# Kernel optimization log

Hardware: AMD Instinct MI355X
Metric: run time of the kernel (lower is better)

Reference implementation:

```python
import math
import jax, jax.numpy as jnp
import numpy as np

B, T, H = 4096, 49, 512

def setup_inputs() -> dict:
    key = jax.random.key(0)
    ks = jax.random.split(key, 13)
    sc = 1.0 / math.sqrt(H)
    return {
        "v": jax.random.normal(ks[0], (B, T, H), dtype=jnp.float32),
        "h": jax.random.normal(ks[1], (B, H), dtype=jnp.float32),
        "s": jax.random.normal(ks[2], (B, H), dtype=jnp.float32),
        "W_h": jax.random.normal(ks[3], (H, H), dtype=jnp.float32) * sc,
        "b_h": jax.random.normal(ks[4], (H,), dtype=jnp.float32) * sc,
        "W_v": jax.random.normal(ks[5], (H, H), dtype=jnp.float32) * sc,
        "b_v": jax.random.normal(ks[6], (H,), dtype=jnp.float32) * sc,
        "w_z": jax.random.normal(ks[7], (H,), dtype=jnp.float32) * sc,
        "b_z": jax.random.normal(ks[8], (), dtype=jnp.float32) * sc,
        "W_s": jax.random.normal(ks[9], (H, H), dtype=jnp.float32) * sc,
        "b_s": jax.random.normal(ks[10], (H,), dtype=jnp.float32) * sc,
        "w_beta": jax.random.normal(ks[11], (H,), dtype=jnp.float32) * sc,
        "b_beta": jax.random.normal(ks[12], (), dtype=jnp.float32) * sc,
    }

def reference(v, h, s, W_h, b_h, W_v, b_v, w_z, b_z, W_s, b_s, w_beta, b_beta):
    # eval mode: dropout is identity
    h_proj = h @ W_h + b_h                                  # [B, H]
    v_proj = jnp.einsum('bth,hk->btk', v, W_v) + b_v        # [B, T, H]
    z = jnp.tanh(h_proj[:, None, :] + v_proj)               # [B, T, H]
    z = jnp.einsum('bth,h->bt', z, w_z) + b_z               # [B, T]
    beta = jnp.tanh((s @ W_s + b_s + h_proj) * math.sqrt(0.5))  # [B, H]
    beta = (beta @ w_beta + b_beta)[:, None]                # [B, 1]
    a = jax.nn.softmax(jnp.concatenate([z, beta], axis=1), axis=1)  # [B, T+1]
    v_ext = jnp.concatenate([v, s[:, None, :]], axis=1)     # [B, T+1, H]
    c = jnp.einsum('bt,bth->bh', a, v_ext)                  # [B, H]
    return c
```

## Files before the change

kernel.cpp:

```cpp
#include <hip/hip_runtime.h>
#include <stdint.h>

#define B_ 4096
#define T_ 49
#define H_ 512
#define BT_ (B_*T_)
#define BB 16

typedef __bf16 bf16x8 __attribute__((ext_vector_type(8)));
typedef float  f32x4  __attribute__((ext_vector_type(4)));
typedef unsigned short ushort_;

__device__ __forceinline__ ushort_ f2bf(float f){
  unsigned int u = __float_as_uint(f);
  u += 0x7fffu + ((u >> 16) & 1u);
  return (ushort_)(u >> 16);
}

__device__ __forceinline__ float fast_tanh(float x){
  float e = __expf(2.0f * x);
  return 1.0f - 2.0f * __builtin_amdgcn_rcpf(e + 1.0f);
}

__global__ __launch_bounds__(256) void k_pack(const float* __restrict__ W,
                                              ushort_* __restrict__ pack){
  int idx = blockIdx.x * 256 + threadIdx.x;
  int lane = idx & 63;
  int gt   = (idx >> 6) & 31;
  int kk   = idx >> 11;
  int col  = gt*16 + (lane & 15);
  int k0   = kk*32 + (lane >> 4)*8;
  ushort4 lo, hi;
  lo.x = f2bf(W[(k0+0)*H_ + col]);
  lo.y = f2bf(W[(k0+1)*H_ + col]);
  lo.z = f2bf(W[(k0+2)*H_ + col]);
  lo.w = f2bf(W[(k0+3)*H_ + col]);
  hi.x = f2bf(W[(k0+4)*H_ + col]);
  hi.y = f2bf(W[(k0+5)*H_ + col]);
  hi.z = f2bf(W[(k0+6)*H_ + col]);
  hi.w = f2bf(W[(k0+7)*H_ + col]);
  ushort4* dst = (ushort4*)pack;
  dst[idx*2]   = lo;
  dst[idx*2+1] = hi;
}

__global__ __launch_bounds__(256) void k_proj2(
    const float* __restrict__ h, const float* __restrict__ s,
    const ushort_* __restrict__ whp, const ushort_* __restrict__ wsp,
    const float* __restrict__ bh, const float* __restrict__ bs,
    const float* __restrict__ bv, const float* __restrict__ wbeta,
    const float* __restrict__ bbeta_p,
    float* __restrict__ hpb, float* __restrict__ beta)
{
  __shared__ __align__(16) ushort_ hl[16*H_];
  __shared__ __align__(16) ushort_ sl[16*H_];
  __shared__ float zwp[4][16];
  const int tid = threadIdx.x;
  const int w = tid >> 6, lane = tid & 63;
  const int l15 = lane & 15, l4 = lane >> 4;
  const int b0 = blockIdx.x * 16;

  {
    const int r = tid >> 4;
    const float4* hsrc = (const float4*)(h + (size_t)(b0+r)*H_);
    const float4* ssrc = (const float4*)(s + (size_t)(b0+r)*H_);
    #pragma unroll
    for(int p=0;p<8;p++){
      int q  = (tid & 15) + p*16;
      int k0 = q*4;
      float4 fh = hsrc[q];
      float4 fs = ssrc[q];
      int idx = (k0>>5)*512 + ((((k0&31)>>3)<<4) + r)*8 + (k0&7);
      ushort4 uh; uh.x=f2bf(fh.x); uh.y=f2bf(fh.y); uh.z=f2bf(fh.z); uh.w=f2bf(fh.w);
      ushort4 us; us.x=f2bf(fs.x); us.y=f2bf(fs.y); us.z=f2bf(fs.z); us.w=f2bf(fs.w);
      *(ushort4*)&hl[idx] = uh;
      *(ushort4*)&sl[idx] = us;
    }
  }
  __syncthreads();

  const bf16x8* __restrict__ bph = (const bf16x8*)whp;
  const bf16x8* __restrict__ bps = (const bf16x8*)wsp;
  const int bbase = w*512 + lane;

  f32x4 acch[8], accs[8];
  #pragma unroll
  for(int ni=0;ni<8;ni++){ acch[ni]=(f32x4){0,0,0,0}; accs[ni]=(f32x4){0,0,0,0}; }

  #pragma unroll 2
  for(int kk=0;kk<16;kk++){
    bf16x8 ah = *(const bf16x8*)&hl[kk*512 + lane*8];
    bf16x8 as2 = *(const bf16x8*)&sl[kk*512 + lane*8];
    #pragma unroll
    for(int ni=0;ni<8;ni++){
      acch[ni] = __builtin_amdgcn_mfma_f32_16x16x32_bf16(ah,  bph[kk*2048 + bbase + ni*64], acch[ni], 0,0,0);
      accs[ni] = __builtin_amdgcn_mfma_f32_16x16x32_bf16(as2, bps[kk*2048 + bbase + ni*64], accs[ni], 0,0,0);
    }
  }

  float bhv[8], bsv[8], bvv[8], wbv[8];
  #pragma unroll
  for(int ni=0;ni<8;ni++){
    int col = w*128 + ni*16 + l15;
    bhv[ni] = bh[col]; bsv[ni] = bs[col]; bvv[ni] = bv[col]; wbv[ni] = wbeta[col];
  }
  float btsum[4];
  #pragma unroll
  for(int rr=0;rr<4;rr++){
    int row = l4*4 + rr;
    float bsum = 0.f;
    #pragma unroll
    for(int ni=0;ni<8;ni++){
      int col = w*128 + ni*16 + l15;
      float hp = acch[ni][rr] + bhv[ni];
      hpb[(size_t)(b0+row)*H_ + col] = hp + bvv[ni];
      float bt = fast_tanh((accs[ni][rr] + bsv[ni] + hp) * 0.70710678118654752f);
      bsum = fmaf(bt, wbv[ni], bsum);
    }
    btsum[rr] = bsum;
  }
  #pragma unroll
  for(int rr=0;rr<4;rr++){
    btsum[rr] += __shfl_xor(btsum[rr], 1);
    btsum[rr] += __shfl_xor(btsum[rr], 2);
    btsum[rr] += __shfl_xor(btsum[rr], 4);
    btsum[rr] += __shfl_xor(btsum[rr], 8);
    if(l15 == 0) zwp[w][l4*4+rr] = btsum[rr];
  }
  __syncthreads();
  if(tid < 16)
    beta[b0+tid] = zwp[0][tid] + zwp[1][tid] + zwp[2][tid] + zwp[3][tid] + bbeta_p[0];
}

__global__ __launch_bounds__(256, 2) void k_fused(
    const float* __restrict__ v, const ushort_* __restrict__ bpack,
    const float* __restrict__ hpb, const float* __restrict__ wz,
    const float* __restrict__ bz_p, const float* __restrict__ beta,
    const float* __restrict__ s, float* __restrict__ out)
{
  __shared__ __align__(16) ushort_ Av[49*512];
  __shared__ float zw[4][64];
  __shared__ float a_s[64];
  const int tid = threadIdx.x;
  const int w = tid >> 6, lane = tid & 63;
  const int l15 = lane & 15, l4 = lane >> 4;
  const int b = blockIdx.x;

  const f32x4* __restrict__ vsrc = (const f32x4*)(v + (size_t)b * T_ * H_);
  const bf16x8* __restrict__ bp = (const bf16x8*)bpack;
  const int bbase = w*256 + lane;

  const int srow = tid >> 4, c4 = tid & 15;
  const int slot = ((c4 >> 1) ^ (srow & 7));
  const int wsub = ((c4 & 1) << 3);
  const bool r48 = (tid < 16);

#define VLOAD(N0,N1,N2,N3, CH) { \
    N0 = __builtin_nontemporal_load(vsrc + (srow     )*128 + (CH)*16 + c4); \
    N1 = __builtin_nontemporal_load(vsrc + (srow + 16)*128 + (CH)*16 + c4); \
    N2 = __builtin_nontemporal_load(vsrc + (srow + 32)*128 + (CH)*16 + c4); \
    if(r48) N3 = __builtin_nontemporal_load(vsrc + 48*128 + (CH)*16 + c4); }

#define SWRITE(N0,N1,N2,N3, CH) { \
    const int cb_ = (CH)*128; ushort4 u_; \
    u_.x=f2bf(N0[0]); u_.y=f2bf(N0[1]); u_.z=f2bf(N0[2]); u_.w=f2bf(N0[3]); \
    *(ushort4*)((char*)Av + (srow   )*1024 + cb_ + (slot<<4) + wsub) = u_; \
    u_.x=f2bf(N1[0]); u_.y=f2bf(N1[1]); u_.z=f2bf(N1[2]); u_.w=f2bf(N1[3]); \
    *(ushort4*)((char*)Av + (srow+16)*1024 + cb_ + (slot<<4) + wsub) = u_; \
    u_.x=f2bf(N2[0]); u_.y=f2bf(N2[1]); u_.z=f2bf(N2[2]); u_.w=f2bf(N2[3]); \
    *(ushort4*)((char*)Av + (srow+32)*1024 + cb_ + (slot<<4) + wsub) = u_; \
    if(r48){ \
      u_.x=f2bf(N3[0]); u_.y=f2bf(N3[1]); u_.z=f2bf(N3[2]); u_.w=f2bf(N3[3]); \
      *(ushort4*)((char*)Av + 48*1024 + cb_ + (slot<<4) + wsub) = u_; } }

#define AFRAG(af, KS) { \
    _Pragma("unroll") \
    for(int mi=0;mi<4;mi++){ \
      int row_ = (mi < 3) ? (mi*16 + l15) : 48; \
      int g_   = ((KS)*4 + l4) ^ (row_ & 7); \
      af[mi] = *(const bf16x8*)((const char*)Av + row_*1024 + (g_<<4)); } }

#define MFMA16(af, bfr) { \
    __builtin_amdgcn_s_setprio(1); \
    _Pragma("unroll") \
    for(int mi=0;mi<4;mi++) \
      _Pragma("unroll") \
      for(int ni=0;ni<4;ni++) \
        acc[mi][ni] = __builtin_amdgcn_mfma_f32_16x16x32_bf16(af[mi], bfr[ni], acc[mi][ni], 0,0,0); \
    __builtin_amdgcn_s_setprio(0); }

  f32x4 A0,A1,A2,A3, B0,B1,B2,B3;
  f32x4 acc[4][4];
  #pragma unroll
  for(int mi=0;mi<4;mi++)
    #pragma unroll
    for(int ni=0;ni<4;ni++) acc[mi][ni] = (f32x4){0.f,0.f,0.f,0.f};

  VLOAD(A0,A1,A2,A3, 0)
  SWRITE(A0,A1,A2,A3, 0)
  VLOAD(A0,A1,A2,A3, 1)
  VLOAD(B0,B1,B2,B3, 2)

  bf16x8 ba[4], bb[4], af[4];
  #pragma unroll
  for(int ni=0;ni<4;ni++) ba[ni] = bp[bbase + ni*64];
  __syncthreads();

#define BODY(C, W0,W1,W2,W3) { \
    _Pragma("unroll") \
    for(int ni=0;ni<4;ni++) bb[ni] = bp[(2*(C)+1)*2048 + bbase + ni*64]; \
    AFRAG(af, 2*(C)) \
    MFMA16(af, ba) \
    if((C) < 7){ SWRITE(W0,W1,W2,W3, (C)+1) } \
    if((C) < 5){ VLOAD(W0,W1,W2,W3, (C)+3) } \
    if((C) < 7){ \
      _Pragma("unroll") \
      for(int ni=0;ni<4;ni++) ba[ni] = bp[(2*(C)+2)*2048 + bbase + ni*64]; } \
    AFRAG(af, 2*(C)+1) \
    MFMA16(af, bb) \
    __syncthreads(); }

  #pragma unroll 1
  for(int cc=0; cc<4; cc++){
    const int c0 = 2*cc;
    BODY(c0,   A0,A1,A2,A3)
    BODY(c0+1, B0,B1,B2,B3)
  }

  {
    float wzv[4], hp0[4];
    #pragma unroll
    for(int ni=0;ni<4;ni++){
      int col = w*64 + ni*16 + l15;
      wzv[ni] = wz[col];
      hp0[ni] = hpb[(size_t)b*H_ + col];
    }
    float zp[16];
    #pragma unroll
    for(int mi=0;mi<4;mi++)
      #pragma unroll
      for(int r=0;r<4;r++){
        float az = 0.f;
        #pragma unroll
        for(int ni=0;ni<4;ni++)
          az = fmaf(fast_tanh(acc[mi][ni][r] + hp0[ni]), wzv[ni], az);
        zp[mi*4+r] = az;
      }
    #pragma unroll
    for(int i=0;i<16;i++){
      zp[i] += __shfl_xor(zp[i], 1);
      zp[i] += __shfl_xor(zp[i], 2);
      zp[i] += __shfl_xor(zp[i], 4);
      zp[i] += __shfl_xor(zp[i], 8);
    }
    if(l15 == 0){
      #pragma unroll
      for(int mi=0;mi<4;mi++)
        #pragma unroll
        for(int r=0;r<4;r++)
          zw[w][mi*16 + l4*4 + r] = zp[mi*4+r];
    }
  }

  #pragma unroll
  for(int mi=0;mi<4;mi++)
    #pragma unroll
    for(int ni=0;ni<4;ni++) acc[mi][ni] = (f32x4){0.f,0.f,0.f,0.f};

  #pragma unroll
  for(int ni=0;ni<4;ni++) ba[ni] = bp[1024 + bbase + ni*64];

  #pragma unroll 1
  for(int k2=0;k2<8;k2++){
    #pragma unroll
    for(int ni=0;ni<4;ni++) bb[ni] = bp[(2*k2+1)*2048 + 1024 + bbase + ni*64];
    AFRAG(af, 2*k2)
    MFMA16(af, ba)
    if(k2 < 7){
      #pragma unroll
      for(int ni=0;ni<4;ni++) ba[ni] = bp[(2*k2+2)*2048 + 1024 + bbase + ni*64];
    }
    AFRAG(af, 2*k2+1)
    MFMA16(af, bb)
  }

  {
    float wzv[4], hp0[4];
    #pragma unroll
    for(int ni=0;ni<4;ni++){
      int col = 256 + w*64 + ni*16 + l15;
      wzv[ni] = wz[col];
      hp0[ni] = hpb[(size_t)b*H_ + col];
    }
    float zp[16];
    #pragma unroll
    for(int mi=0;mi<4;mi++)
      #pragma unroll
      for(int r=0;r<4;r++){
        float az = 0.f;
        #pragma unroll
        for(int ni=0;ni<4;ni++)
          az = fmaf(fast_tanh(acc[mi][ni][r] + hp0[ni]), wzv[ni], az);
        zp[mi*4+r] = az;
      }
    #pragma unroll
    for(int i=0;i<16;i++){
      zp[i] += __shfl_xor(zp[i], 1);
      zp[i] += __shfl_xor(zp[i], 2);
      zp[i] += __shfl_xor(zp[i], 4);
      zp[i] += __shfl_xor(zp[i], 8);
    }
    if(l15 == 0){
      #pragma unroll
      for(int mi=0;mi<4;mi++)
        #pragma unroll
        for(int r=0;r<4;r++)
          zw[w][mi*16 + l4*4 + r] += zp[mi*4+r];
    }
  }
  __syncthreads();

  if(tid < 64){
    float zv;
    if(tid < T_)       zv = zw[0][tid] + zw[1][tid] + zw[2][tid] + zw[3][tid] + bz_p[0];
    else if(tid == T_) zv = beta[b];
    else               zv = -3.0e38f;
    float m = zv;
    #pragma unroll
    for(int off=32;off>=1;off>>=1) m = fmaxf(m, __shfl_xor(m, off));
    float e = (tid <= T_) ? __expf(zv - m) : 0.f;
    float ssum = e;
    #pragma unroll
    for(int off=32;off>=1;off>>=1) ssum += __shfl_xor(ssum, off);
    a_s[tid] = e * __builtin_amdgcn_rcpf(ssum);
  }
  __syncthreads();

  const int n0 = tid * 2;
  float ax = 0.f, ay = 0.f;
  #pragma unroll 7
  for(int t=0;t<T_;t++){
    float at = a_s[t];
    unsigned int u = *(const unsigned int*)((const char*)Av + t*1024
                       + ((((n0>>3) ^ (t&7)))<<4) + ((n0&7)<<1));
    float x = __uint_as_float((u & 0xFFFFu) << 16);
    float y = __uint_as_float(u & 0xFFFF0000u);
    ax = fmaf(at, x, ax);
    ay = fmaf(at, y, ay);
  }
  float a49 = a_s[T_];
  float2 sv = ((const float2*)(s + (size_t)b*H_))[tid];
  ax = fmaf(a49, sv.x, ax);
  ay = fmaf(a49, sv.y, ay);
  float2 res; res.x = ax; res.y = ay;
  ((float2*)(out + (size_t)b*H_))[tid] = res;
}

extern "C" void kernel_launch(void* const* d_in, const int* in_sizes, int n_in,
                              void* d_out, int out_size, void* d_ws, size_t ws_size,
                              hipStream_t stream)
{
  const float* v   = (const float*)d_in[0];
  const float* h   = (const float*)d_in[1];
  const float* s   = (const float*)d_in[2];
  const float* Wh  = (const float*)d_in[3];
  const float* bh  = (const float*)d_in[4];
  const float* Wv  = (const float*)d_in[5];
  const float* bv  = (const float*)d_in[6];
  const float* wz  = (const float*)d_in[7];
  const float* bz  = (const float*)d_in[8];
  const float* Ws  = (const float*)d_in[9];
  const float* bs  = (const float*)d_in[10];
  const float* wb  = (const float*)d_in[11];
  const float* bbet= (const float*)d_in[12];
  float* out = (float*)d_out;

  float* hpb  = (float*)d_ws;
  float* beta = hpb + (size_t)B_*H_;
  ushort_* bpack = (ushort_*)(beta + B_);
  ushort_* whp   = bpack + (size_t)H_*H_;
  ushort_* wsp   = whp   + (size_t)H_*H_;

  k_pack <<<128, 256, 0, stream>>>(Wv, bpack);
  k_pack <<<128, 256, 0, stream>>>(Wh, whp);
  k_pack <<<128, 256, 0, stream>>>(Ws, wsp);
  k_proj2<<<B_/16, 256, 0, stream>>>(h, s, whp, wsp, bh, bs, bv, wb, bbet, hpb, beta);
  k_fused<<<B_, 256, 0, stream>>>(v, bpack, hpb, wz, bz, beta, s, out);
}
```

Measured before the change: 239.0 us.

## Stage whole v tile into LDS upfront and raise occupancy to three blocks

The first GEMM pass no longer overlaps v loads and LDS writes with MFMA work. The full 49x512 tile is loaded and converted to bf16 into shared memory before any matrix math, which removes the per-chunk __syncthreads. Launch bounds now request three blocks per CU, so latency is hidden by more resident waves rather than software pipelining. The risks are tighter register limits, possible spills, and LDS capacity: about 49KB per block times three must fit.

After: 218.0 us. -8.8%, faster.

```diff
diff --git a/kernel.cpp b/kernel.cpp
--- a/kernel.cpp
+++ b/kernel.cpp
@@ -132,7 +132,7 @@
     beta[b0+tid] = zwp[0][tid] + zwp[1][tid] + zwp[2][tid] + zwp[3][tid] + bbeta_p[0];
 }
 
-__global__ __launch_bounds__(256, 2) void k_fused(
+__global__ __launch_bounds__(256, 3) void k_fused(
     const float* __restrict__ v, const ushort_* __restrict__ bpack,
     const float* __restrict__ hpb, const float* __restrict__ wz,
     const float* __restrict__ bz_p, const float* __restrict__ beta,
@@ -189,42 +189,41 @@
         acc[mi][ni] = __builtin_amdgcn_mfma_f32_16x16x32_bf16(af[mi], bfr[ni], acc[mi][ni], 0,0,0); \
     __builtin_amdgcn_s_setprio(0); }
 
-  f32x4 A0,A1,A2,A3, B0,B1,B2,B3;
+  {
+    f32x4 A0,A1,A2,A3, B0,B1,B2,B3;
+    VLOAD(A0,A1,A2,A3, 0)
+    #pragma unroll
+    for(int cc=0; cc<4; cc++){
+      VLOAD(B0,B1,B2,B3, 2*cc+1)
+      SWRITE(A0,A1,A2,A3, 2*cc)
+      if(cc < 3) VLOAD(A0,A1,A2,A3, 2*cc+2)
+      SWRITE(B0,B1,B2,B3, 2*cc+1)
+    }
+  }
+
   f32x4 acc[4][4];
   #pragma unroll
   for(int mi=0;mi<4;mi++)
     #pragma unroll
     for(int ni=0;ni<4;ni++) acc[mi][ni] = (f32x4){0.f,0.f,0.f,0.f};
 
-  VLOAD(A0,A1,A2,A3, 0)
-  SWRITE(A0,A1,A2,A3, 0)
-  VLOAD(A0,A1,A2,A3, 1)
-  VLOAD(B0,B1,B2,B3, 2)
-
   bf16x8 ba[4], bb[4], af[4];
   #pragma unroll
   for(int ni=0;ni<4;ni++) ba[ni] = bp[bbase + ni*64];
   __syncthreads();
 
-#define BODY(C, W0,W1,W2,W3) { \
-    _Pragma("unroll") \
-    for(int ni=0;ni<4;ni++) bb[ni] = bp[(2*(C)+1)*2048 + bbase + ni*64]; \
-    AFRAG(af, 2*(C)) \
-    MFMA16(af, ba) \
-    if((C) < 7){ SWRITE(W0,W1,W2,W3, (C)+1) } \
-    if((C) < 5){ VLOAD(W0,W1,W2,W3, (C)+3) } \
-    if((C) < 7){ \
-      _Pragma("unroll") \
-      for(int ni=0;ni<4;ni++) ba[ni] = bp[(2*(C)+2)*2048 + bbase + ni*64]; } \
-    AFRAG(af, 2*(C)+1) \
-    MFMA16(af, bb) \
-    __syncthreads(); }
-
   #pragma unroll 1
-  for(int cc=0; cc<4; cc++){
-    const int c0 = 2*cc;
-    BODY(c0,   A0,A1,A2,A3)
-    BODY(c0+1, B0,B1,B2,B3)
+  for(int kk=0; kk<16; kk+=2){
+    #pragma unroll
+    for(int ni=0;ni<4;ni++) bb[ni] = bp[(kk+1)*2048 + bbase + ni*64];
+    AFRAG(af, kk)
+    MFMA16(af, ba)
+    if(kk < 14){
+      #pragma unroll
+      for(int ni=0;ni<4;ni++) ba[ni] = bp[(kk+2)*2048 + bbase + ni*64];
+    }
+    AFRAG(af, kk+1)
+    MFMA16(af, bb)
   }
 
   {
@@ -271,16 +270,16 @@
   for(int ni=0;ni<4;ni++) ba[ni] = bp[1024 + bbase + ni*64];
 
   #pragma unroll 1
-  for(int k2=0;k2<8;k2++){
-    #pragma unroll
-    for(int ni=0;ni<4;ni++) bb[ni] = bp[(2*k2+1)*2048 + 1024 + bbase + ni*64];
-    AFRAG(af, 2*k2)
+  for(int kk=0; kk<16; kk+=2){
+    #pragma unroll
+    for(int ni=0;ni<4;ni++) bb[ni] = bp[(kk+1)*2048 + 1024 + bbase + ni*64];
+    AFRAG(af, kk)
     MFMA16(af, ba)
-    if(k2 < 7){
-      #pragma unroll
-      for(int ni=0;ni<4;ni++) ba[ni] = bp[(2*k2+2)*2048 + 1024 + bbase + ni*64];
-    }
-    AFRAG(af, 2*k2+1)
+    if(kk < 14){
+      #pragma unroll
+      for(int ni=0;ni<4;ni++) ba[ni] = bp[(kk+2)*2048 + 1024 + bbase + ni*64];
+    }
+    AFRAG(af, kk+1)
     MFMA16(af, bb)
   }
 
```
